# Optimization experiments

Measured on AMD Instinct MI355X. Metric: run time of the kernel, lower is better.

Reference implementation:

```python
import jax, jax.numpy as jnp
import numpy as np

N, E, D, H, C, L = 50000, 600000, 128, 128, 64, 3
LN_EPS = 1e-5


def setup_inputs() -> dict:
    key = jax.random.key(0)
    ks = jax.random.split(key, 6)
    x = jax.random.normal(ks[0], (N, D), jnp.float32)
    edge_index = jax.random.randint(ks[1], (2, E), 0, N, jnp.int32)
    Wg = jax.random.normal(ks[2], (L, D, H), jnp.float32) * (1.0 / np.sqrt(D))
    bg = jnp.zeros((L, H), jnp.float32)
    ln_g = jnp.ones((L, H), jnp.float32)
    ln_b = jnp.zeros((L, H), jnp.float32)
    mlp_W1 = jax.random.normal(ks[3], (D + L * H, H), jnp.float32) * (1.0 / np.sqrt(D + L * H))
    mlp_b1 = jnp.zeros((H,), jnp.float32)
    mlp_W2 = jax.random.normal(ks[4], (H, C), jnp.float32) * (1.0 / np.sqrt(H))
    mlp_b2 = jnp.zeros((C,), jnp.float32)
    return {"x": x, "edge_index": edge_index, "Wg": Wg, "bg": bg,
            "ln_g": ln_g, "ln_b": ln_b, "mlp_W1": mlp_W1, "mlp_b1": mlp_b1,
            "mlp_W2": mlp_W2, "mlp_b2": mlp_b2}


def _layer_norm(h, g, b):
    mu = jnp.mean(h, axis=-1, keepdims=True)
    var = jnp.mean((h - mu) ** 2, axis=-1, keepdims=True)
    return g * (h - mu) * jax.lax.rsqrt(var + LN_EPS) + b


def _gcn(h, W, b, src, dst, dinv):
    # GCNConv with added self-loops and symmetric normalization:
    # out = D^{-1/2} (A + I) D^{-1/2} (h W) + b
    hW = h @ W                                   # [N, H]
    coef = (dinv[src] * dinv[dst])[:, None]      # [E, 1]
    agg = jax.ops.segment_sum(hW[src] * coef, dst, num_segments=N)
    agg = agg + hW * (dinv * dinv)[:, None]      # self-loop term
    return agg + b


def reference(x, edge_index, Wg, bg, ln_g, ln_b, mlp_W1, mlp_b1, mlp_W2, mlp_b2):
    src, dst = edge_index[0], edge_index[1]
    # degree including self-loop
    deg = jnp.ones((N,), x.dtype).at[dst].add(1.0)
    dinv = jax.lax.rsqrt(deg)
    feats = [x]
    h = x
    for i in range(L):  # small fixed layer count
        h = _gcn(h, Wg[i], bg[i], src, dst, dinv)
        h = _layer_norm(h, ln_g[i], ln_b[i])
        h = jax.nn.relu(h)
        feats.append(h)
    xc = jnp.concatenate(feats, axis=1)          # [N, D + L*H]
    z = jax.nn.relu(xc @ mlp_W1 + mlp_b1)
    z = z @ mlp_W2 + mlp_b2
    return jax.nn.softmax(z, axis=1)
```

## Files before the change

### kernel.cpp

```cpp
#include <hip/hip_runtime.h>
#include <math.h>

#define D 128
#define HH 128
#define CC 64
#define NLAYERS 3
#define LN_EPS 1e-5f

typedef __attribute__((ext_vector_type(8))) short bf16x8;
typedef __attribute__((ext_vector_type(4))) float f32x4;
typedef unsigned short u16;
typedef unsigned int u32;

__device__ __forceinline__ u16 f2bf(float f) {
    u32 u = __float_as_uint(f);
    u32 r = u + 0x7FFFu + ((u >> 16) & 1u);
    return (u16)(r >> 16);
}
__device__ __forceinline__ float bf2f(u16 h) {
    return __uint_as_float(((u32)h) << 16);
}

__global__ void k_prep(const float* __restrict__ x, u16* __restrict__ xh,
                       const float* __restrict__ Wg, u16* __restrict__ WgtH,
                       const float* __restrict__ W1, u16* __restrict__ W1tH,
                       const float* __restrict__ W2, u16* __restrict__ W2tH,
                       u16* __restrict__ W2tL,
                       int* __restrict__ cnt, int N)
{
    int i = blockIdx.x * blockDim.x + threadIdx.x;
    if (i < N) { cnt[i] = 0; return; }
    i -= N;
    int nx = N * D;
    if (i < nx) {
        int row = i >> 7, c = i & 127;
        xh[(size_t)row * 512 + c] = f2bf(x[i]);
        return;
    }
    i -= nx;
    if (i < NLAYERS * D * HH) {
        int k = i >> 7, n = i & 127;
        int kc = k >> 5, q = (k >> 3) & 3, j = k & 7;
        WgtH[(((kc * 4 + q) << 7) + n) * 8 + j] = f2bf(Wg[i]);
        return;
    }
    i -= NLAYERS * D * HH;
    if (i < (D + NLAYERS * HH) * HH) {
        int k = i >> 7, n = i & 127;
        int kc = k >> 5, q = (k >> 3) & 3, j = k & 7;
        W1tH[(((kc * 4 + q) << 7) + n) * 8 + j] = f2bf(W1[i]);
        return;
    }
    i -= (D + NLAYERS * HH) * HH;
    if (i < HH * CC) {
        int k = i >> 6, n = i & 63;
        int kc = k >> 5, q = (k >> 3) & 3, j = k & 7;
        float v = W2[i];
        u16 h = f2bf(v);
        int o = (((kc * 4 + q) << 6) + n) * 8 + j;
        W2tH[o] = h;
        W2tL[o] = f2bf(v - bf2f(h));
    }
}


__global__ void k_count(const int* __restrict__ dst, int* __restrict__ cnt, int E) {
    int i = blockIdx.x * blockDim.x + threadIdx.x;
    if (i < E) atomicAdd(&cnt[dst[i]], 1);
}

__global__ void k_scan_a(const int* __restrict__ cnt, int* __restrict__ rowptr,
                         int* __restrict__ bsum, int N) {
    __shared__ int s[1024];
    int tid = threadIdx.x;
    int i = blockIdx.x * 1024 + tid;
    int v = (i < N) ? cnt[i] : 0;
    s[tid] = v;
    __syncthreads();
    for (int off = 1; off < 1024; off <<= 1) {
        int t = (tid >= off) ? s[tid - off] : 0;
        __syncthreads();
        s[tid] += t;
        __syncthreads();
    }
    if (i < N) rowptr[i] = s[tid] - v;
    if (tid == 1023) bsum[blockIdx.x] = s[tid];
}

__global__ void k_scan_c(int* __restrict__ rowptr, const int* __restrict__ bsum,
                         const int* __restrict__ cnt, float* __restrict__ dinv,
                         int* __restrict__ cursor, int N, int E, int nsb) {
    __shared__ int sb[64];
    if (threadIdx.x < 64) {
        int t = threadIdx.x;
        int v = (t < nsb) ? bsum[t] : 0;
        int incl = v;
        #pragma unroll
        for (int off = 1; off < 64; off <<= 1) {
            int u = __shfl_up(incl, off, 64);
            if (t >= off) incl += u;
        }
        sb[t] = incl - v;
    }
    __syncthreads();
    int i = blockIdx.x * blockDim.x + threadIdx.x;
    if (i < N) {
        int v = rowptr[i] + sb[i >> 10];
        rowptr[i] = v;
        cursor[i] = v;
        dinv[i] = rsqrtf(1.0f + (float)cnt[i]);
    }
    if (i == 0) rowptr[N] = E;
}

__global__ void k_scatter(const int* __restrict__ src, const int* __restrict__ dst,
                          const float* __restrict__ dinv,
                          int* __restrict__ cursor, int2* __restrict__ ecol, int E) {
    int i = blockIdx.x * blockDim.x + threadIdx.x;
    if (i < E) {
        int s = src[i], d = dst[i];
        int p = atomicAdd(&cursor[d], 1);
        float c = dinv[s] * dinv[d];
        ecol[p] = make_int2(s, __float_as_int(c));
    }
}

__global__ __launch_bounds__(256) void k_gemm_lf(
    const u16* __restrict__ A, int colOff,
    const u16* __restrict__ Bt, u16* __restrict__ OUTb, int N)
{
    const int tid  = threadIdx.x;
    const int lane = tid & 63;
    const int wave = tid >> 6;
    const int wr   = wave & 1;
    const int wc   = wave >> 1;
    const int quad = lane >> 4;
    const int l15  = lane & 15;
    const int row0 = blockIdx.x * 64;

    const u16* pA[2];
    #pragma unroll
    for (int i = 0; i < 2; ++i) {
        int r = row0 + wr * 32 + i * 16 + l15;
        if (r >= N) r = N - 1;
        pA[i] = A + (size_t)r * 512 + colOff + quad * 8;
    }
    const u16* pB = Bt + ((size_t)quad * 128 + wc * 64 + l15) * 8;

    bf16x8 ah[4][2], bh[4][4];
    #pragma unroll
    for (int kc = 0; kc < 4; ++kc) {
        #pragma unroll
        for (int i = 0; i < 2; ++i)
            ah[kc][i] = *(const bf16x8*)(pA[i] + kc * 32);
        #pragma unroll
        for (int j = 0; j < 4; ++j)
            bh[kc][j] = *(const bf16x8*)(pB + (size_t)kc * 4096 + j * 128);
    }

    f32x4 acc[2][4];
    #pragma unroll
    for (int i = 0; i < 2; ++i)
        #pragma unroll
        for (int j = 0; j < 4; ++j)
            #pragma unroll
            for (int r = 0; r < 4; ++r) acc[i][j][r] = 0.f;

    #pragma unroll
    for (int kc = 0; kc < 4; ++kc)
        #pragma unroll
        for (int i = 0; i < 2; ++i)
            #pragma unroll
            for (int j = 0; j < 4; ++j)
                acc[i][j] = __builtin_amdgcn_mfma_f32_16x16x32_bf16(ah[kc][i], bh[kc][j], acc[i][j], 0, 0, 0);

    #pragma unroll
    for (int i = 0; i < 2; ++i)
        #pragma unroll
        for (int j = 0; j < 4; ++j) {
            int col = wc * 64 + j * 16 + l15;
            #pragma unroll
            for (int r = 0; r < 4; ++r) {
                int grow = row0 + wr * 32 + i * 16 + quad * 4 + r;
                if (grow < N)
                    OUTb[(size_t)grow * 128 + col] = f2bf(acc[i][j][r]);
            }
        }
}

__global__ __launch_bounds__(256) void k_mlp_fused(
    const u16* __restrict__ xcH,
    const u16* __restrict__ B1t, const float* __restrict__ b1,
    const u16* __restrict__ W2h, const u16* __restrict__ W2l,
    const float* __restrict__ b2, float* __restrict__ out, int N)
{
    __shared__ float sAcc[32 * 132];
    __shared__ u16 sZh[32 * 128];
    __shared__ u16 sZl[32 * 128];

    const int tid  = threadIdx.x;
    const int lane = tid & 63;
    const int wave = tid >> 6;
    const int wc   = wave & 1;
    const int kg   = wave >> 1;
    const int quad = lane >> 4;
    const int l15  = lane & 15;
    const int row0 = blockIdx.x * 32;

    const u16* pA[2];
    #pragma unroll
    for (int f = 0; f < 2; ++f) {
        int r = row0 + f * 16 + l15;
        if (r >= N) r = N - 1;
        pA[f] = xcH + (size_t)r * 512 + quad * 8;
    }
    const u16* pB = B1t + ((size_t)quad * 128 + wc * 64 + l15) * 8;

    f32x4 acc[2][4];
    #pragma unroll
    for (int f = 0; f < 2; ++f)
        #pragma unroll
        for (int j = 0; j < 4; ++j)
            #pragma unroll
            for (int r = 0; r < 4; ++r) acc[f][j][r] = 0.f;

    bf16x8 abuf[3][2], bbuf[3][4];
    #define LOADI(t, s)                                                          \
        {                                                                        \
            const int g = kg * 8 + (t);                                          \
            _Pragma("unroll")                                                    \
            for (int f = 0; f < 2; ++f)                                          \
                abuf[s][f] = *(const bf16x8*)(pA[f] + g * 32);                   \
            _Pragma("unroll")                                                    \
            for (int j = 0; j < 4; ++j)                                          \
                bbuf[s][j] = *(const bf16x8*)(pB + (size_t)g * 4096 + j * 128);  \
        }
    LOADI(0, 0)
    LOADI(1, 1)
    #pragma unroll
    for (int t = 0; t < 8; ++t) {
        if (t + 2 < 8) {
            const int s = (t + 2) % 3;
            LOADI(t + 2, s)
        }
        const int u = t % 3;
        #pragma unroll
        for (int f = 0; f < 2; ++f)
            #pragma unroll
            for (int j = 0; j < 4; ++j)
                acc[f][j] = __builtin_amdgcn_mfma_f32_16x16x32_bf16(abuf[u][f], bbuf[u][j], acc[f][j], 0, 0, 0);
    }
    #undef LOADI

    if (kg == 1) {
        #pragma unroll
        for (int f = 0; f < 2; ++f)
            #pragma unroll
            for (int jt = 0; jt < 4; ++jt) {
                int col = wc * 64 + jt * 16 + l15;
                #pragma unroll
                for (int r = 0; r < 4; ++r) {
                    int row = f * 16 + quad * 4 + r;
                    sAcc[row * 132 + col] = acc[f][jt][r];
                }
            }
    }
    __syncthreads();
    if (kg == 0) {
        #pragma unroll
        for (int jt = 0; jt < 4; ++jt) {
            int col = wc * 64 + jt * 16 + l15;
            float bv = b1[col];
            int qq = col >> 3, jj = col & 7;
            #pragma unroll
            for (int f = 0; f < 2; ++f) {
                #pragma unroll
                for (int rr = 0; rr < 4; ++rr) {
                    int row = f * 16 + quad * 4 + rr;
                    float v = fmaxf(acc[f][jt][rr] + sAcc[row * 132 + col] + bv, 0.f);
                    u16 h = f2bf(v);
                    sZh[(qq * 32 + row) * 8 + jj] = h;
                    sZl[(qq * 32 + row) * 8 + jj] = f2bf(v - bf2f(h));
                }
            }
        }
    }
    __syncthreads();

    if (kg == 0) {
        f32x4 oacc[4];
        #pragma unroll
        for (int j = 0; j < 4; ++j)
            #pragma unroll
            for (int r = 0; r < 4; ++r) oacc[j][r] = 0.f;

        #pragma unroll
        for (int kc = 0; kc < 4; ++kc) {
            int qq = kc * 4 + quad;
            bf16x8 zh = *(const bf16x8*)&sZh[(qq * 32 + wc * 16 + l15) * 8];
            bf16x8 zl = *(const bf16x8*)&sZl[(qq * 32 + wc * 16 + l15) * 8];
            #pragma unroll
            for (int jt = 0; jt < 4; ++jt) {
                int n = jt * 16 + l15;
                bf16x8 wh = *(const bf16x8*)&W2h[(qq * 64 + n) * 8];
                bf16x8 wl = *(const bf16x8*)&W2l[(qq * 64 + n) * 8];
                oacc[jt] = __builtin_amdgcn_mfma_f32_16x16x32_bf16(zh, wh, oacc[jt], 0, 0, 0);
                oacc[jt] = __builtin_amdgcn_mfma_f32_16x16x32_bf16(zh, wl, oacc[jt], 0, 0, 0);
                oacc[jt] = __builtin_amdgcn_mfma_f32_16x16x32_bf16(zl, wh, oacc[jt], 0, 0, 0);
            }
        }

        #pragma unroll
        for (int jt = 0; jt < 4; ++jt) {
            float bv = b2[jt * 16 + l15];
            #pragma unroll
            for (int r = 0; r < 4; ++r) oacc[jt][r] += bv;
        }
        #pragma unroll
        for (int r = 0; r < 4; ++r) {
            float m = fmaxf(fmaxf(oacc[0][r], oacc[1][r]), fmaxf(oacc[2][r], oacc[3][r]));
            #pragma unroll
            for (int mask = 8; mask; mask >>= 1) m = fmaxf(m, __shfl_xor(m, mask, 64));
            float p0 = __expf(oacc[0][r] - m);
            float p1 = __expf(oacc[1][r] - m);
            float p2 = __expf(oacc[2][r] - m);
            float p3 = __expf(oacc[3][r] - m);
            float s = p0 + p1 + p2 + p3;
            #pragma unroll
            for (int mask = 8; mask; mask >>= 1) s += __shfl_xor(s, mask, 64);
            float inv = 1.0f / s;
            int grow = row0 + wc * 16 + quad * 4 + r;
            if (grow < N) {
                float* o = out + (size_t)grow * CC + l15;
                o[0]  = p0 * inv;
                o[16] = p1 * inv;
                o[32] = p2 * inv;
                o[48] = p3 * inv;
            }
        }
    }
}

__global__ __launch_bounds__(256, 8) void k_agg_ln(
    const u16* __restrict__ hWb,
    const int* __restrict__ rowptr, const int2* __restrict__ ecol,
    const float* __restrict__ dinv,
    const float* __restrict__ bg, const float* __restrict__ g,
    const float* __restrict__ b,
    u16* __restrict__ outHi, int N)
{
    const int lane = threadIdx.x & 63;
    const int f0 = lane * 2;

    const float bgx = bg[f0], bgy = bg[f0 + 1];
    const float gx  = g[f0],  gy  = g[f0 + 1];
    const float bx  = b[f0],  by  = b[f0 + 1];

    const int nwaves = gridDim.x * 4;
    for (int wid = blockIdx.x * 4 + (threadIdx.x >> 6); wid < N; wid += nwaves) {
        float di = dinv[wid];
        float sc = di * di;

        u32 hv = *(const u32*)(hWb + (size_t)wid * HH + f0);
        float ax  = bf2f((u16)hv) * sc;
        float ay  = bf2f((u16)(hv >> 16)) * sc;
        float ax1 = 0.f, ay1 = 0.f, ax2 = 0.f, ay2 = 0.f, ax3 = 0.f, ay3 = 0.f;

        int e0 = rowptr[wid];
        int e1 = rowptr[wid + 1];
        int e = e0;
        for (; e + 8 <= e1; e += 8) {
            int2 p[8];
            u32  v[8];
            #pragma unroll
            for (int t = 0; t < 8; ++t) p[t] = ecol[e + t];
            #pragma unroll
            for (int t = 0; t < 8; ++t)
                v[t] = *(const u32*)(hWb + (size_t)p[t].x * HH + f0);
            #pragma unroll
            for (int t = 0; t < 8; ++t) {
                float c = __int_as_float(p[t].y);
                float vx = bf2f((u16)v[t]) * c;
                float vy = bf2f((u16)(v[t] >> 16)) * c;
                switch (t & 3) {
                    case 0: ax  += vx; ay  += vy; break;
                    case 1: ax1 += vx; ay1 += vy; break;
                    case 2: ax2 += vx; ay2 += vy; break;
                    default: ax3 += vx; ay3 += vy; break;
                }
            }
        }
        for (; e + 4 <= e1; e += 4) {
            int2 p0 = ecol[e];
            int2 p1 = ecol[e + 1];
            int2 p2 = ecol[e + 2];
            int2 p3 = ecol[e + 3];
            u32 v0 = *(const u32*)(hWb + (size_t)p0.x * HH + f0);
            u32 v1 = *(const u32*)(hWb + (size_t)p1.x * HH + f0);
            u32 v2 = *(const u32*)(hWb + (size_t)p2.x * HH + f0);
            u32 v3 = *(const u32*)(hWb + (size_t)p3.x * HH + f0);
            ax  += bf2f((u16)v0) * __int_as_float(p0.y);  ay  += bf2f((u16)(v0 >> 16)) * __int_as_float(p0.y);
            ax1 += bf2f((u16)v1) * __int_as_float(p1.y);  ay1 += bf2f((u16)(v1 >> 16)) * __int_as_float(p1.y);
            ax2 += bf2f((u16)v2) * __int_as_float(p2.y);  ay2 += bf2f((u16)(v2 >> 16)) * __int_as_float(p2.y);
            ax3 += bf2f((u16)v3) * __int_as_float(p3.y);  ay3 += bf2f((u16)(v3 >> 16)) * __int_as_float(p3.y);
        }
        for (; e < e1; ++e) {
            int2 p = ecol[e];
            u32 v = *(const u32*)(hWb + (size_t)p.x * HH + f0);
            float c = __int_as_float(p.y);
            ax += bf2f((u16)v) * c;
            ay += bf2f((u16)(v >> 16)) * c;
        }
        ax += ax1 + ax2 + ax3;
        ay += ay1 + ay2 + ay3;
        ax += bgx;
        ay += bgy;

        float ssum = ax + ay;
        #pragma unroll
        for (int off = 32; off; off >>= 1) ssum += __shfl_xor(ssum, off, 64);
        float mu = ssum * (1.0f / 128.0f);
        float dx = ax - mu, dy = ay - mu;
        float vsum = dx * dx + dy * dy;
        #pragma unroll
        for (int off = 32; off; off >>= 1) vsum += __shfl_xor(vsum, off, 64);
        float rstd = rsqrtf(vsum * (1.0f / 128.0f) + LN_EPS);

        float ox = fmaxf(gx * dx * rstd + bx, 0.f);
        float oy = fmaxf(gy * dy * rstd + by, 0.f);

        *(u32*)&outHi[(size_t)wid * 512 + f0] = (u32)f2bf(ox) | ((u32)f2bf(oy) << 16);
    }
}

extern "C" void kernel_launch(void* const* d_in, const int* in_sizes, int n_in,
                              void* d_out, int out_size, void* d_ws, size_t ws_size,
                              hipStream_t stream) {
    const float* x   = (const float*)d_in[0];
    const int*   ei  = (const int*)  d_in[1];
    const float* Wg  = (const float*)d_in[2];
    const float* bg  = (const float*)d_in[3];
    const float* lng = (const float*)d_in[4];
    const float* lnb = (const float*)d_in[5];
    const float* W1  = (const float*)d_in[6];
    const float* b1  = (const float*)d_in[7];
    const float* W2  = (const float*)d_in[8];
    const float* b2  = (const float*)d_in[9];
    float* out = (float*)d_out;

    const int N = in_sizes[0] / D;
    const int E = in_sizes[1] / 2;
    const int* srcp = ei;
    const int* dstp = ei + E;

    char* ws = (char*)d_ws;
    size_t off = 0;
    auto alloc = [&](size_t bytes) -> void* {
        void* p = ws + off;
        off += (bytes + 511) & ~(size_t)511;
        return p;
    };
    int*   cnt    = (int*)  alloc((size_t)N * 4);
    int*   rowptr = (int*)  alloc((size_t)(N + 1) * 4);
    int*   cursor = (int*)  alloc((size_t)N * 4);
    int*   bsum   = (int*)  alloc(64 * 4);
    int2*  ecol   = (int2*) alloc((size_t)E * 8);
    float* dinv   = (float*)alloc((size_t)N * 4);
    u16*   hWb    = (u16*)  alloc((size_t)N * HH * 2);
    u16*   xcH    = (u16*)  alloc((size_t)N * 512 * 2);
    u16*   WgtH   = (u16*)  alloc((size_t)NLAYERS * D * HH * 2);
    u16*   W1tH   = (u16*)  alloc((size_t)(D + NLAYERS * HH) * HH * 2);
    u16*   W2tH   = (u16*)  alloc((size_t)HH * CC * 2);
    u16*   W2tL   = (u16*)  alloc((size_t)HH * CC * 2);

    const int B = 256;
    const int gE = (E + B - 1) / B;
    const int nsb = (N + 1023) / 1024;

    const int prepTotal = N + N * D + NLAYERS * D * HH
                        + (D + NLAYERS * HH) * HH + HH * CC;
    k_prep<<<(prepTotal + B - 1) / B, B, 0, stream>>>(x, xcH, Wg, WgtH, W1, W1tH,
                                                      W2, W2tH, W2tL, cnt, N);
    k_count<<<gE, B, 0, stream>>>(dstp, cnt, E);
    k_scan_a<<<nsb, 1024, 0, stream>>>(cnt, rowptr, bsum, N);
    k_scan_c<<<(N + B - 1) / B, B, 0, stream>>>(rowptr, bsum, cnt, dinv, cursor, N, E, nsb);
    k_scatter<<<gE, B, 0, stream>>>(srcp, dstp, dinv, cursor, ecol, E);

    const int gemmBlocks = (N + 63) / 64;
    const int mlpBlocks  = (N + 31) / 32;
    const int aggBlocks  = 2048;

    for (int l = 0; l < NLAYERS; ++l) {
        k_gemm_lf<<<gemmBlocks, B, 0, stream>>>(xcH, l * HH,
                                                WgtH + (size_t)l * D * HH, hWb, N);
        k_agg_ln<<<aggBlocks, B, 0, stream>>>(hWb, rowptr, ecol, dinv,
                                              bg + (size_t)l * HH,
                                              lng + (size_t)l * HH,
                                              lnb + (size_t)l * HH,
                                              xcH + (size_t)(l + 1) * HH, N);
    }

    k_mlp_fused<<<mlpBlocks, B, 0, stream>>>(xcH, W1tH, b1,
                                             W2tH, W2tL, b2, out, N);
}
```

Measured before the change: 317.4 us.

## Fuse CSR build into cooperative kernel, split edges across half-waves in aggregation

Replaces the four CSR-building kernels (count, two scan passes, scatter) with a single cooperative kernel that uses grid-wide syncs, removing launch gaps between them. The x-to-bf16 conversion in prep is vectorised to float4 loads. The aggregation kernel now splits each node's edges between the two half-waves, each lane handling 4 features with 8-byte gathers, and combines the halves with one cross-half shuffle. The cooperative launch needs all 1024 blocks to be resident at once, and the wider gathers change the memory access pattern.

```diff
diff --git a/kernel.cpp b/kernel.cpp
--- a/kernel.cpp
+++ b/kernel.cpp
@@ -1,5 +1,8 @@
 #include <hip/hip_runtime.h>
+#include <hip/hip_cooperative_groups.h>
 #include <math.h>
+
+namespace cg = cooperative_groups;
 
 #define D 128
 #define HH 128
@@ -25,19 +28,19 @@
                        const float* __restrict__ Wg, u16* __restrict__ WgtH,
                        const float* __restrict__ W1, u16* __restrict__ W1tH,
                        const float* __restrict__ W2, u16* __restrict__ W2tH,
-                       u16* __restrict__ W2tL,
-                       int* __restrict__ cnt, int N)
+                       u16* __restrict__ W2tL, int N)
 {
     int i = blockIdx.x * blockDim.x + threadIdx.x;
-    if (i < N) { cnt[i] = 0; return; }
-    i -= N;
-    int nx = N * D;
-    if (i < nx) {
-        int row = i >> 7, c = i & 127;
-        xh[(size_t)row * 512 + c] = f2bf(x[i]);
+    int nx4 = N * (D / 4);
+    if (i < nx4) {
+        float4 v = *(const float4*)(x + (size_t)i * 4);
+        int row = i >> 5, c = (i & 31) << 2;
+        ushort4 o;
+        o.x = f2bf(v.x); o.y = f2bf(v.y); o.z = f2bf(v.z); o.w = f2bf(v.w);
+        *(ushort4*)&xh[(size_t)row * 512 + c] = o;
         return;
     }
-    i -= nx;
+    i -= nx4;
     if (i < NLAYERS * D * HH) {
         int k = i >> 7, n = i & 127;
         int kc = k >> 5, q = (k >> 3) & 3, j = k & 7;
@@ -63,65 +66,74 @@
     }
 }
 
-
-__global__ void k_count(const int* __restrict__ dst, int* __restrict__ cnt, int E) {
-    int i = blockIdx.x * blockDim.x + threadIdx.x;
-    if (i < E) atomicAdd(&cnt[dst[i]], 1);
-}
-
-__global__ void k_scan_a(const int* __restrict__ cnt, int* __restrict__ rowptr,
-                         int* __restrict__ bsum, int N) {
-    __shared__ int s[1024];
-    int tid = threadIdx.x;
-    int i = blockIdx.x * 1024 + tid;
-    int v = (i < N) ? cnt[i] : 0;
-    s[tid] = v;
-    __syncthreads();
-    for (int off = 1; off < 1024; off <<= 1) {
-        int t = (tid >= off) ? s[tid - off] : 0;
+__global__ __launch_bounds__(256) void k_csr(
+    const int* __restrict__ src, const int* __restrict__ dst,
+    int* __restrict__ cnt, int* __restrict__ rowptr, int* __restrict__ bsum,
+    int* __restrict__ cursor, float* __restrict__ dinv,
+    int2* __restrict__ ecol, int N, int E)
+{
+    cg::grid_group grid = cg::this_grid();
+    __shared__ int s[256];
+    __shared__ int carry;
+    const int tid = threadIdx.x;
+    const int gsz = gridDim.x * 256;
+    const int gi  = blockIdx.x * 256 + tid;
+    const int nch = (N + 255) >> 8;
+
+    for (int i = gi; i < N; i += gsz) cnt[i] = 0;
+    grid.sync();
+    for (int i = gi; i < E; i += gsz) atomicAdd(&cnt[dst[i]], 1);
+    grid.sync();
+    for (int ch = blockIdx.x; ch < nch; ch += gridDim.x) {
+        int i = (ch << 8) + tid;
+        int v = (i < N) ? cnt[i] : 0;
+        s[tid] = v;
         __syncthreads();
-        s[tid] += t;
+        for (int off = 1; off < 256; off <<= 1) {
+            int t = (tid >= off) ? s[tid - off] : 0;
+            __syncthreads();
+            s[tid] += t;
+            __syncthreads();
+        }
+        if (i < N) rowptr[i] = s[tid] - v;
+        if (tid == 255) bsum[ch] = s[tid];
         __syncthreads();
     }
-    if (i < N) rowptr[i] = s[tid] - v;
-    if (tid == 1023) bsum[blockIdx.x] = s[tid];
-}
-
-__global__ void k_scan_c(int* __restrict__ rowptr, const int* __restrict__ bsum,
-                         const int* __restrict__ cnt, float* __restrict__ dinv,
-                         int* __restrict__ cursor, int N, int E, int nsb) {
-    __shared__ int sb[64];
-    if (threadIdx.x < 64) {
-        int t = threadIdx.x;
-        int v = (t < nsb) ? bsum[t] : 0;
-        int incl = v;
-        #pragma unroll
-        for (int off = 1; off < 64; off <<= 1) {
-            int u = __shfl_up(incl, off, 64);
-            if (t >= off) incl += u;
-        }
-        sb[t] = incl - v;
-    }
-    __syncthreads();
-    int i = blockIdx.x * blockDim.x + threadIdx.x;
-    if (i < N) {
-        int v = rowptr[i] + sb[i >> 10];
+    grid.sync();
+    if (blockIdx.x == 0) {
+        if (tid == 0) carry = 0;
+        __syncthreads();
+        for (int base = 0; base < nch; base += 256) {
+            int idx = base + tid;
+            int v = (idx < nch) ? bsum[idx] : 0;
+            s[tid] = v;
+            __syncthreads();
+            for (int off = 1; off < 256; off <<= 1) {
+                int t = (tid >= off) ? s[tid - off] : 0;
+                __syncthreads();
+                s[tid] += t;
+                __syncthreads();
+            }
+            if (idx < nch) bsum[idx] = carry + s[tid] - v;
+            __syncthreads();
+            if (tid == 0) carry += s[255];
+            __syncthreads();
+        }
+    }
+    grid.sync();
+    for (int i = gi; i < N; i += gsz) {
+        int v = rowptr[i] + bsum[i >> 8];
         rowptr[i] = v;
         cursor[i] = v;
         dinv[i] = rsqrtf(1.0f + (float)cnt[i]);
     }
-    if (i == 0) rowptr[N] = E;
-}
-
-__global__ void k_scatter(const int* __restrict__ src, const int* __restrict__ dst,
-                          const float* __restrict__ dinv,
-                          int* __restrict__ cursor, int2* __restrict__ ecol, int E) {
-    int i = blockIdx.x * blockDim.x + threadIdx.x;
-    if (i < E) {
-        int s = src[i], d = dst[i];
+    if (gi == 0) rowptr[N] = E;
+    grid.sync();
+    for (int i = gi; i < E; i += gsz) {
+        int s0 = src[i], d = dst[i];
         int p = atomicAdd(&cursor[d], 1);
-        float c = dinv[s] * dinv[d];
-        ecol[p] = make_int2(s, __float_as_int(c));
+        float c = dinv[s0] * dinv[d];
+        ecol[p] = make_int2(s0, __float_as_int(c));
     }
 }
 
@@ -350,86 +362,87 @@
     u16* __restrict__ outHi, int N)
 {
     const int lane = threadIdx.x & 63;
-    const int f0 = lane * 2;
-
-    const float bgx = bg[f0], bgy = bg[f0 + 1];
-    const float gx  = g[f0],  gy  = g[f0 + 1];
-    const float bx  = b[f0],  by  = b[f0 + 1];
+    const int h    = lane >> 5;
+    const int c0   = (lane & 31) << 2;
+
+    const float4 bgv = *(const float4*)(bg + c0);
+    const float4 gv  = *(const float4*)(g + c0);
+    const float4 bv  = *(const float4*)(b + c0);
 
     const int nwaves = gridDim.x * 4;
     for (int wid = blockIdx.x * 4 + (threadIdx.x >> 6); wid < N; wid += nwaves) {
         float di = dinv[wid];
-        float sc = di * di;
-
-        u32 hv = *(const u32*)(hWb + (size_t)wid * HH + f0);
-        float ax  = bf2f((u16)hv) * sc;
-        float ay  = bf2f((u16)(hv >> 16)) * sc;
-        float ax1 = 0.f, ay1 = 0.f, ax2 = 0.f, ay2 = 0.f, ax3 = 0.f, ay3 = 0.f;
+        float sc = (h == 0) ? di * di : 0.f;
+
+        uint2 hv = *(const uint2*)(hWb + (size_t)wid * HH + c0);
+        float a0 = bf2f((u16)hv.x) * sc;
+        float a1 = bf2f((u16)(hv.x >> 16)) * sc;
+        float a2 = bf2f((u16)hv.y) * sc;
+        float a3 = bf2f((u16)(hv.y >> 16)) * sc;
+        float q0 = 0.f, q1 = 0.f, q2 = 0.f, q3 = 0.f;
 
         int e0 = rowptr[wid];
-        int e1 = rowptr[wid + 1];
-        int e = e0;
-        for (; e + 8 <= e1; e += 8) {
-            int2 p[8];
-            u32  v[8];
-            #pragma unroll
-            for (int t = 0; t < 8; ++t) p[t] = ecol[e + t];
-            #pragma unroll
-            for (int t = 0; t < 8; ++t)
-                v[t] = *(const u32*)(hWb + (size_t)p[t].x * HH + f0);
-            #pragma unroll
-            for (int t = 0; t < 8; ++t) {
+        int m  = rowptr[wid + 1] - e0;
+        int ch = (m - h + 1) >> 1;
+        const int2* ep = ecol + e0 + h;
+
+        int k = 0;
+        for (; k + 4 <= ch; k += 4) {
+            int2 p[4];
+            uint2 v[4];
+            #pragma unroll
+            for (int t = 0; t < 4; ++t) p[t] = ep[2 * (k + t)];
+            #pragma unroll
+            for (int t = 0; t < 4; ++t)
+                v[t] = *(const uint2*)(hWb + (size_t)p[t].x * HH + c0);
+            #pragma unroll
+            for (int t = 0; t < 4; ++t) {
                 float c = __int_as_float(p[t].y);
-                float vx = bf2f((u16)v[t]) * c;
-                float vy = bf2f((u16)(v[t] >> 16)) * c;
-                switch (t & 3) {
-                    case 0: ax  += vx; ay  += vy; break;
-                    case 1: ax1 += vx; ay1 += vy; break;
-                    case 2: ax2 += vx; ay2 += vy; break;
-                    default: ax3 += vx; ay3 += vy; break;
-                }
-            }
-        }
-        for (; e + 4 <= e1; e += 4) {
-            int2 p0 = ecol[e];
-            int2 p1 = ecol[e + 1];
-            int2 p2 = ecol[e + 2];
-            int2 p3 = ecol[e + 3];
-            u32 v0 = *(const u32*)(hWb + (size_t)p0.x * HH + f0);
-            u32 v1 = *(const u32*)(hWb + (size_t)p1.x * HH + f0);
-            u32 v2 = *(const u32*)(hWb + (size_t)p2.x * HH + f0);
-            u32 v3 = *(const u32*)(hWb + (size_t)p3.x * HH + f0);
-            ax  += bf2f((u16)v0) * __int_as_float(p0.y);  ay  += bf2f((u16)(v0 >> 16)) * __int_as_float(p0.y);
-            ax1 += bf2f((u16)v1) * __int_as_float(p1.y);  ay1 += bf2f((u16)(v1 >> 16)) * __int_as_float(p1.y);
-            ax2 += bf2f((u16)v2) * __int_as_float(p2.y);  ay2 += bf2f((u16)(v2 >> 16)) * __int_as_float(p2.y);
-            ax3 += bf2f((u16)v3) * __int_as_float(p3.y);  ay3 += bf2f((u16)(v3 >> 16)) * __int_as_float(p3.y);
-        }
-        for (; e < e1; ++e) {
-            int2 p = ecol[e];
-            u32 v = *(const u32*)(hWb + (size_t)p.x * HH + f0);
+                float x0 = bf2f((u16)v[t].x) * c;
+                float x1 = bf2f((u16)(v[t].x >> 16)) * c;
+                float x2 = bf2f((u16)v[t].y) * c;
+                float x3 = bf2f((u16)(v[t].y >> 16)) * c;
+                if (t & 1) { q0 += x0; q1 += x1; q2 += x2; q3 += x3; }
+                else       { a0 += x0; a1 += x1; a2 += x2; a3 += x3; }
+            }
+        }
+        for (; k < ch; ++k) {
+            int2 p = ep[2 * k];
+            uint2 v = *(const uint2*)(hWb + (size_t)p.x * HH + c0);
             float c = __int_as_float(p.y);
-            ax += bf2f((u16)v) * c;
-            ay += bf2f((u16)(v >> 16)) * c;
-        }
-        ax += ax1 + ax2 + ax3;
-        ay += ay1 + ay2 + ay3;
-        ax += bgx;
-        ay += bgy;
-
-        float ssum = ax + ay;
-        #pragma unroll
-        for (int off = 32; off; off >>= 1) ssum += __shfl_xor(ssum, off, 64);
+            a0 += bf2f((u16)v.x) * c;
+            a1 += bf2f((u16)(v.x >> 16)) * c;
+            a2 += bf2f((u16)v.y) * c;
+            a3 += bf2f((u16)(v.y >> 16)) * c;
+        }
+        a0 += q0; a1 += q1; a2 += q2; a3 += q3;
+
+        a0 += __shfl_xor(a0, 32, 64);
+        a1 += __shfl_xor(a1, 32, 64);
+        a2 += __shfl_xor(a2, 32, 64);
+        a3 += __shfl_xor(a3, 32, 64);
+        a0 += bgv.x; a1 += bgv.y; a2 += bgv.z; a3 += bgv.w;
+
+        float ssum = (a0 + a1) + (a2 + a3);
+        #pragma unroll
+        for (int off = 16; off; off >>= 1) ssum += __shfl_xor(ssum, off, 64);
         float mu = ssum * (1.0f / 128.0f);
-        float dx = ax - mu, dy = ay - mu;
-        float vsum = dx * dx + dy * dy;
-        #pragma unroll
-        for (int off = 32; off; off >>= 1) vsum += __shfl_xor(vsum, off, 64);
+        float d0 = a0 - mu, d1 = a1 - mu, d2 = a2 - mu, d3 = a3 - mu;
+        float vsum = (d0 * d0 + d1 * d1) + (d2 * d2 + d3 * d3);
+        #pragma unroll
+        for (int off = 16; off; off >>= 1) vsum += __shfl_xor(vsum, off, 64);
         float rstd = rsqrtf(vsum * (1.0f / 128.0f) + LN_EPS);
 
-        float ox = fmaxf(gx * dx * rstd + bx, 0.f);
-        float oy = fmaxf(gy * dy * rstd + by, 0.f);
-
-        *(u32*)&outHi[(size_t)wid * 512 + f0] = (u32)f2bf(ox) | ((u32)f2bf(oy) << 16);
+        if (!h) {
+            float o0 = fmaxf(gv.x * d0 * rstd + bv.x, 0.f);
+            float o1 = fmaxf(gv.y * d1 * rstd + bv.y, 0.f);
+            float o2 = fmaxf(gv.z * d2 * rstd + bv.z, 0.f);
+            float o3 = fmaxf(gv.w * d3 * rstd + bv.w, 0.f);
+            uint2 o;
+            o.x = (u32)f2bf(o0) | ((u32)f2bf(o1) << 16);
+            o.y = (u32)f2bf(o2) | ((u32)f2bf(o3) << 16);
+            *(uint2*)&outHi[(size_t)wid * 512 + c0] = o;
+        }
     }
 }
 
@@ -463,7 +476,7 @@
     int*   cnt    = (int*)  alloc((size_t)N * 4);
     int*   rowptr = (int*)  alloc((size_t)(N + 1) * 4);
     int*   cursor = (int*)  alloc((size_t)N * 4);
-    int*   bsum   = (int*)  alloc(64 * 4);
+    int*   bsum   = (int*)  alloc((size_t)((N + 255) / 256 + 1) * 4);
     int2*  ecol   = (int2*) alloc((size_t)E * 8);
     float* dinv   = (float*)alloc((size_t)N * 4);
     u16*   hWb    = (u16*)  alloc((size_t)N * HH * 2);
@@ -474,17 +487,20 @@
     u16*   W2tL   = (u16*)  alloc((size_t)HH * CC * 2);
 
     const int B = 256;
-    const int gE = (E + B - 1) / B;
-    const int nsb = (N + 1023) / 1024;
-
-    const int prepTotal = N + N * D + NLAYERS * D * HH
+
+    const int prepTotal = N * (D / 4) + NLAYERS * D * HH
                         + (D + NLAYERS * HH) * HH + HH * CC;
     k_prep<<<(prepTotal + B - 1) / B, B, 0, stream>>>(x, xcH, Wg, WgtH, W1, W1tH,
-                                                      W2, W2tH, W2tL, cnt, N);
-    k_count<<<gE, B, 0, stream>>>(dstp, cnt, E);
-    k_scan_a<<<nsb, 1024, 0, stream>>>(cnt, rowptr, bsum, N);
-    k_scan_c<<<(N + B - 1) / B, B, 0, stream>>>(rowptr, bsum, cnt, dinv, cursor, N, E, nsb);
-    k_scatter<<<gE, B, 0, stream>>>(srcp, dstp, dinv, cursor, ecol, E);
+                                                      W2, W2tH, W2tL, N);
+
+    {
+        int N_ = N, E_ = E;
+        void* cargs[] = { (void*)&srcp, (void*)&dstp, (void*)&cnt, (void*)&rowptr,
+                          (void*)&bsum, (void*)&cursor, (void*)&dinv, (void*)&ecol,
+                          (void*)&N_, (void*)&E_ };
+        hipLaunchCooperativeKernel((const void*)k_csr, dim3(1024), dim3(B),
+                                   cargs, 0, stream);
+    }
 
     const int gemmBlocks = (N + 63) / 64;
     const int mlpBlocks  = (N + 31) / 32;
```

New measurement: 795.9 us. +150.7%, slower.
